# Optimization experiments

Hardware: AMD Instinct MI355X
Metric: run time of the kernel (lower is better)

The kernel has to match this reference:

```python
import jax, jax.numpy as jnp
import numpy as np

B, S, NH, HD = 2, 4096, 16, 64


def setup_inputs() -> dict:
    key = jax.random.key(0)
    kq, kk, kv = jax.random.split(key, 3)
    q = jax.random.normal(kq, (B, S, NH, HD), dtype=jnp.float32)
    k = jax.random.normal(kk, (B, S, NH, HD), dtype=jnp.float32)
    v = jax.random.normal(kv, (B, S, NH, HD), dtype=jnp.float32)
    return {"q": q, "k": k, "v": v}


def reference(q, k, v):
    # SDPA.__call__ with attention_mask=None, segment_ids=None, is_causal=True, dropout=identity
    q_len, nheads, kv_len = q.shape[-3], q.shape[-2], k.shape[-3]
    qs = q / jnp.sqrt(jnp.asarray(q.shape[-1], q.dtype))
    scores = jnp.einsum('...tnh,...snh->...tns', qs, k)  # [B, q, nheads, kv]
    # causal mask: tril over (q, kv), broadcast over heads axis (-2)
    causal = jnp.tril(jnp.ones((q_len, kv_len), dtype=jnp.bool_))[:, None, :]
    neg_inf = jnp.finfo(scores.dtype).min
    scores = jnp.where(causal, scores, neg_inf)
    weights = jax.nn.softmax(scores.astype(jnp.float32), axis=-1).astype(scores.dtype)
    attn = jnp.einsum('...tns,...snh->...tnh', weights, v)
    return attn
```

## Files before the change

### kernel.cpp

```cpp
#include <hip/hip_runtime.h>


constexpr int BATCH  = 2;
constexpr int SEQ    = 4096;
constexpr int NHEADS = 16;
constexpr int HDIM   = 64;
constexpr int ROWSTR = NHEADS * HDIM;
constexpr int BM     = 128;
constexpr int BN     = 64;
constexpr int QTILES = SEQ / BM;
constexpr int BH     = BATCH * NHEADS;

typedef __attribute__((ext_vector_type(8)))  short v8s;
typedef __attribute__((ext_vector_type(16))) float v16f;
typedef __attribute__((ext_vector_type(4)))  unsigned int v4u;
typedef __attribute__((ext_vector_type(2)))  unsigned int v2u;
typedef __attribute__((ext_vector_type(2)))  __bf16 v2bf;

__device__ __forceinline__ unsigned pkbf(float a, float b) {
#if __has_builtin(__builtin_amdgcn_cvt_pk_bf16_f32)
    return __builtin_bit_cast(unsigned, __builtin_amdgcn_cvt_pk_bf16_f32(a, b));
#else
    unsigned ua = __float_as_uint(a); ua += 0x7FFFu + ((ua >> 16) & 1u);
    unsigned ub = __float_as_uint(b); ub += 0x7FFFu + ((ub >> 16) & 1u);
    return (ua >> 16) | (ub & 0xFFFF0000u);
#endif
}

__device__ __forceinline__ int fswz(int r) { return (r & 7) ^ ((r >> 3) & 3); }

__device__ __forceinline__ void async16(const unsigned short* g, unsigned short* l) {
    __builtin_amdgcn_global_load_lds(
        (const __attribute__((address_space(1))) unsigned int*)g,
        (__attribute__((address_space(3))) unsigned int*)l, 16, 0, 0);
}

__global__ __launch_bounds__(256, 4)
void prep(const float* __restrict__ kf, const float* __restrict__ vf,
          unsigned short* __restrict__ kb, unsigned short* __restrict__ vt)
{
    __shared__ unsigned int lds[128 * 33];
    const int tid = threadIdx.x;
    const int blk = (int)blockIdx.x;

    if (blk < 1024) {
        const float4* src = (const float4*)kf + (size_t)blk * 2048;
        unsigned int* dst = (unsigned int*)kb + (size_t)blk * 4096;
        #pragma unroll
        for (int i = 0; i < 8; ++i) {
            const int n = i * 256 + tid;
            float4 f = src[n];
            *(v2u*)(dst + (size_t)n * 2) = (v2u){pkbf(f.x, f.y), pkbf(f.z, f.w)};
        }
        return;
    }

    const int t  = blk - 1024;
    const int b  = t >> 9;
    const int h  = (t >> 5) & 15;
    const int s0 = (t & 31) * 128;

    {
        const float4* vff = (const float4*)vf + (size_t)b * SEQ * 256;
        const int c2 = (tid & 15) * 2;
        #pragma unroll
        for (int i = 0; i < 8; ++i) {
            const int srow = i * 16 + (tid >> 4);
            float4 f = vff[(size_t)(s0 + srow) * 256 + h * 16 + (tid & 15)];
            lds[srow * 33 + c2]     = pkbf(f.x, f.y);
            lds[srow * 33 + c2 + 1] = pkbf(f.z, f.w);
        }
    }
    __syncthreads();
    {
        const int w    = tid >> 6;
        const int lane = tid & 63;
        const int sh   = (lane & 1) * 16;
        const unsigned int* lcol = &lds[w * 32 * 33 + (lane >> 1)];
        unsigned int out[16];
        #pragma unroll
        for (int j = 0; j < 16; ++j) {
            const unsigned a = lcol[(2 * j)     * 33];
            const unsigned c = lcol[(2 * j + 1) * 33];
            out[j] = ((a >> sh) & 0xFFFFu) | (((c >> sh) & 0xFFFFu) << 16);
        }
        unsigned int* dst = (unsigned int*)vt
            + ((size_t)((b * NHEADS + h) * HDIM + lane)) * (SEQ / 2)
            + ((s0 + w * 32) >> 1);
        #pragma unroll
        for (int j = 0; j < 4; ++j)
            *(v4u*)(dst + 4 * j) = (v4u){out[4*j], out[4*j+1], out[4*j+2], out[4*j+3]};
    }
}

__global__ __launch_bounds__(256, 4)
void fa_fwd(const float* __restrict__ qf, const unsigned short* __restrict__ kb,
            const unsigned short* __restrict__ vt, float* __restrict__ og)
{
    __shared__ __align__(16) unsigned short k_s[2][64 * 64];
    __shared__ __align__(16) unsigned short v_s[2][64 * 64];

    const int tid  = threadIdx.x;
    const int wave = tid >> 6;
    const int lane = tid & 63;
    const int hh   = lane >> 5;
    const int l32  = lane & 31;

    const int n  = (int)blockIdx.x;
    const int qtile = QTILES - 1 - (n >> 5);
    const int bh = n & 31;
    const int b = bh >> 4, h = bh & 15;
    const int qbase = qtile * BM;
    const int jmax  = 2 * qtile + 2;

    const int lrow  = lane >> 3;
    const int lcol8 = (lane & 7) ^ lrow ^ wave;
    const int fx = (l32 & 7) ^ ((l32 >> 3) & 3);

    {
        const int krow = tid >> 2;
        const int kc   = (tid & 3) * 16;
        const int sg0  = (2 * (tid & 3))     ^ fswz(krow);
        const int sg1  = (2 * (tid & 3) + 1) ^ fswz(krow);
        const float sc = 0.125f * 1.44269504088896340736f;
        #pragma unroll
        for (int half = 0; half < 2; ++half) {
            const float4* src = (const float4*)(qf +
                ((size_t)((b * SEQ + qbase + half * 64 + krow) * NHEADS + h)) * HDIM + kc);
            float4 f0 = src[0], f1 = src[1], f2 = src[2], f3 = src[3];
            unsigned short* dst = half ? &v_s[0][krow * 64] : &k_s[0][krow * 64];
            *(v4u*)&dst[sg0 * 8] = (v4u){pkbf(f0.x*sc, f0.y*sc), pkbf(f0.z*sc, f0.w*sc),
                                         pkbf(f1.x*sc, f1.y*sc), pkbf(f1.z*sc, f1.w*sc)};
            *(v4u*)&dst[sg1 * 8] = (v4u){pkbf(f2.x*sc, f2.y*sc), pkbf(f2.z*sc, f2.w*sc),
                                         pkbf(f3.x*sc, f3.y*sc), pkbf(f3.z*sc, f3.w*sc)};
        }
    }
    __syncthreads();
    v8s bq[4];
    {
        const int R = wave * 32 + l32;
        const unsigned short* qrow = (R < 64) ? &k_s[0][R * 64] : &v_s[0][(R - 64) * 64];
        #pragma unroll
        for (int c = 0; c < 4; ++c)
            bq[c] = *(const v8s*)&qrow[(((2*c + hh) ^ fswz(R & 63)) * 8)];
    }
    __syncthreads();

    const unsigned short* kgb = kb + (size_t)b * SEQ * ROWSTR + (size_t)h * HDIM;
    const unsigned short* vgb = vt + (size_t)bh * HDIM * SEQ;

    #pragma unroll
    for (int i = 0; i < 2; ++i) {
        const int rbase = i * 32 + wave * 8;
        async16(kgb + (size_t)(rbase + lrow) * ROWSTR + lcol8 * 8, &k_s[0][rbase * 64]);
        async16(vgb + (size_t)(rbase + lrow) * SEQ    + lcol8 * 8, &v_s[0][rbase * 64]);
    }

    v16f o_acc[2];
    o_acc[0] = (v16f)(0.f); o_acc[1] = (v16f)(0.f);
    float l_lane = 0.f;
    const int q_abs = qbase + wave * 32 + l32;

#if __has_builtin(__builtin_amdgcn_fdot2_f32_bf16)
    const v2bf ones2 = __builtin_bit_cast(v2bf, 0x3F803F80u);
#endif

    for (int jt = 0; jt < jmax; ++jt) {
        const int buf = jt & 1;
        __syncthreads();

        if (jt + 1 < jmax) {
            const int nb  = (jt + 1) & 1;
            const int kb2 = (jt + 1) * BN;
            #pragma unroll
            for (int i = 0; i < 2; ++i) {
                const int rbase = i * 32 + wave * 8;
                async16(kgb + (size_t)(kb2 + rbase + lrow) * ROWSTR + lcol8 * 8, &k_s[nb][rbase * 64]);
                async16(vgb + (size_t)(rbase + lrow) * SEQ + kb2    + lcol8 * 8, &v_s[nb][rbase * 64]);
            }
        }

        v16f sacc[2];
        sacc[0] = (v16f)(0.f); sacc[1] = (v16f)(0.f);
        __builtin_amdgcn_s_setprio(1);
        #pragma unroll
        for (int mt = 0; mt < 2; ++mt) {
            const int r = mt * 32 + l32;
            #pragma unroll
            for (int c = 0; c < 4; ++c) {
                v8s ak = *(const v8s*)&k_s[buf][r * 64 + (((2*c + hh) ^ fx) * 8)];
                sacc[mt] = __builtin_amdgcn_mfma_f32_32x32x16_bf16(ak, bq[c], sacc[mt], 0, 0, 0);
            }
        }
        __builtin_amdgcn_s_setprio(0);

        const bool masked = (jt >= jmax - 2);
        v8s pf[4];
        #pragma unroll
        for (int mt = 0; mt < 2; ++mt) {
            #pragma unroll
            for (int r = 0; r < 16; ++r) {
                float pv = __builtin_amdgcn_exp2f(sacc[mt][r]);
                if (masked) {
                    const int k_abs = jt * 64 + mt * 32 + (r & 3) + 8 * (r >> 2) + 4 * hh;
                    pv = (k_abs > q_abs) ? 0.f : pv;
                }
                sacc[mt][r] = pv;
#if !__has_builtin(__builtin_amdgcn_fdot2_f32_bf16)
                l_lane += pv;
#endif
            }
            #pragma unroll
            for (int cc = 0; cc < 2; ++cc) {
                const unsigned lo0 = pkbf(sacc[mt][8*cc+0], sacc[mt][8*cc+1]);
                const unsigned lo1 = pkbf(sacc[mt][8*cc+2], sacc[mt][8*cc+3]);
                const unsigned hi0 = pkbf(sacc[mt][8*cc+4], sacc[mt][8*cc+5]);
                const unsigned hi1 = pkbf(sacc[mt][8*cc+6], sacc[mt][8*cc+7]);
#if __has_builtin(__builtin_amdgcn_fdot2_f32_bf16)
                l_lane = __builtin_amdgcn_fdot2_f32_bf16(__builtin_bit_cast(v2bf, lo0), ones2, l_lane, false);
                l_lane = __builtin_amdgcn_fdot2_f32_bf16(__builtin_bit_cast(v2bf, lo1), ones2, l_lane, false);
                l_lane = __builtin_amdgcn_fdot2_f32_bf16(__builtin_bit_cast(v2bf, hi0), ones2, l_lane, false);
                l_lane = __builtin_amdgcn_fdot2_f32_bf16(__builtin_bit_cast(v2bf, hi1), ones2, l_lane, false);
#endif
#if __has_builtin(__builtin_amdgcn_permlane32_swap)
                auto r0 = __builtin_amdgcn_permlane32_swap(lo0, hi0, false, false);
                auto r1 = __builtin_amdgcn_permlane32_swap(lo1, hi1, false, false);
                pf[mt*2 + cc] = __builtin_bit_cast(v8s, (v4u){r0[0], r1[0], r0[1], r1[1]});
#else
                const unsigned s0 = hh ? lo0 : hi0;
                const unsigned s1 = hh ? lo1 : hi1;
                const unsigned t0 = (unsigned)__shfl_xor((int)s0, 32, 64);
                const unsigned t1 = (unsigned)__shfl_xor((int)s1, 32, 64);
                v4u w;
                w.x = hh ? t0 : lo0;
                w.y = hh ? t1 : lo1;
                w.z = hh ? hi0 : t0;
                w.w = hh ? hi1 : t1;
                pf[mt*2 + cc] = __builtin_bit_cast(v8s, w);
#endif
            }
        }

        __builtin_amdgcn_s_setprio(1);
        #pragma unroll
        for (int nt = 0; nt < 2; ++nt) {
            const int r = nt * 32 + l32;
            #pragma unroll
            for (int c = 0; c < 4; ++c) {
                v8s bv = *(const v8s*)&v_s[buf][r * 64 + (((2*c + hh) ^ fx) * 8)];
                o_acc[nt] = __builtin_amdgcn_mfma_f32_32x32x16_bf16(pf[c], bv, o_acc[nt], 0, 0, 0);
            }
        }
        __builtin_amdgcn_s_setprio(0);
    }

    const float lt = l_lane + __shfl_xor(l_lane, 32);

    #pragma unroll
    for (int r = 0; r < 16; ++r) {
        const int q_local = (r & 3) + 8 * (r >> 2) + 4 * hh;
        const float inv_l = 1.0f / __shfl(lt, q_local, 32);
        const int qrow = qbase + wave * 32 + q_local;
        float* dst = og + ((size_t)((b * SEQ + qrow) * NHEADS + h)) * HDIM + l32;
        dst[0]  = o_acc[0][r] * inv_l;
        dst[32] = o_acc[1][r] * inv_l;
    }
}

extern "C" void kernel_launch(void* const* d_in, const int* in_sizes, int n_in,
                              void* d_out, int out_size, void* d_ws, size_t ws_size,
                              hipStream_t stream) {
    const float* q = (const float*)d_in[0];
    const float* k = (const float*)d_in[1];
    const float* v = (const float*)d_in[2];
    float* out = (float*)d_out;

    const size_t TEN = (size_t)BATCH * NHEADS * SEQ * HDIM;
    unsigned short* kbuf = (unsigned short*)d_ws;
    unsigned short* vbuf = kbuf + TEN;

    prep<<<2048, 256, 0, stream>>>(k, v, kbuf, vbuf);
    fa_fwd<<<QTILES * BH, 256, 0, stream>>>(q, kbuf, vbuf, out);
}
```

Before: 242.6 us.

## Double query tile to 256 rows with 8 waves per block sharing K/V tiles

```diff
diff --git a/kernel.cpp b/kernel.cpp
--- a/kernel.cpp
+++ b/kernel.cpp
@@ -6,7 +6,7 @@
 constexpr int NHEADS = 16;
 constexpr int HDIM   = 64;
 constexpr int ROWSTR = NHEADS * HDIM;
-constexpr int BM     = 128;
+constexpr int BM     = 256;
 constexpr int BN     = 64;
 constexpr int QTILES = SEQ / BM;
 constexpr int BH     = BATCH * NHEADS;
@@ -93,7 +93,7 @@
     }
 }
 
-__global__ __launch_bounds__(256, 4)
+__global__ __launch_bounds__(512, 2)
 void fa_fwd(const float* __restrict__ qf, const unsigned short* __restrict__ kb,
             const unsigned short* __restrict__ vt, float* __restrict__ og)
 {
@@ -111,24 +111,30 @@
     const int bh = n & 31;
     const int b = bh >> 4, h = bh & 15;
     const int qbase = qtile * BM;
-    const int jmax  = 2 * qtile + 2;
+    const int jmax  = 4 * qtile + 4;
 
     const int lrow  = lane >> 3;
-    const int lcol8 = (lane & 7) ^ lrow ^ wave;
+    const int lcol8 = (lane & 7) ^ lrow ^ (wave & 3);
     const int fx = (l32 & 7) ^ ((l32 >> 3) & 3);
 
     {
         const int krow = tid >> 2;
         const int kc   = (tid & 3) * 16;
-        const int sg0  = (2 * (tid & 3))     ^ fswz(krow);
-        const int sg1  = (2 * (tid & 3) + 1) ^ fswz(krow);
         const float sc = 0.125f * 1.44269504088896340736f;
         #pragma unroll
         for (int half = 0; half < 2; ++half) {
+            const int row = half * 128 + krow;
+            const int rr  = row & 63;
+            const int sg0 = (2 * (tid & 3))     ^ fswz(rr);
+            const int sg1 = (2 * (tid & 3) + 1) ^ fswz(rr);
             const float4* src = (const float4*)(qf +
-                ((size_t)((b * SEQ + qbase + half * 64 + krow) * NHEADS + h)) * HDIM + kc);
+                ((size_t)((b * SEQ + qbase + row) * NHEADS + h)) * HDIM + kc);
             float4 f0 = src[0], f1 = src[1], f2 = src[2], f3 = src[3];
-            unsigned short* dst = half ? &v_s[0][krow * 64] : &k_s[0][krow * 64];
+            const int sel = row >> 6;
+            unsigned short* dst = (sel == 0) ? &k_s[0][rr * 64]
+                                : (sel == 1) ? &k_s[1][rr * 64]
+                                : (sel == 2) ? &v_s[0][rr * 64]
+                                             : &v_s[1][rr * 64];
             *(v4u*)&dst[sg0 * 8] = (v4u){pkbf(f0.x*sc, f0.y*sc), pkbf(f0.z*sc, f0.w*sc),
                                          pkbf(f1.x*sc, f1.y*sc), pkbf(f1.z*sc, f1.w*sc)};
             *(v4u*)&dst[sg1 * 8] = (v4u){pkbf(f2.x*sc, f2.y*sc), pkbf(f2.z*sc, f2.w*sc),
@@ -138,24 +144,29 @@
     __syncthreads();
     v8s bq[4];
     {
-        const int R = wave * 32 + l32;
-        const unsigned short* qrow = (R < 64) ? &k_s[0][R * 64] : &v_s[0][(R - 64) * 64];
+        const int R   = wave * 32 + l32;
+        const int sel = wave >> 1;
+        const int rr  = R & 63;
+        const unsigned short* qb = (sel == 0) ? &k_s[0][0]
+                                 : (sel == 1) ? &k_s[1][0]
+                                 : (sel == 2) ? &v_s[0][0]
+                                              : &v_s[1][0];
         #pragma unroll
         for (int c = 0; c < 4; ++c)
-            bq[c] = *(const v8s*)&qrow[(((2*c + hh) ^ fswz(R & 63)) * 8)];
+            bq[c] = *(const v8s*)&qb[rr * 64 + (((2*c + hh) ^ fswz(rr)) * 8)];
     }
     __syncthreads();
 
     const unsigned short* kgb = kb + (size_t)b * SEQ * ROWSTR + (size_t)h * HDIM;
     const unsigned short* vgb = vt + (size_t)bh * HDIM * SEQ;
 
-    #pragma unroll
-    for (int i = 0; i < 2; ++i) {
-        const int rbase = i * 32 + wave * 8;
+    {
+        const int rbase = wave * 8;
         async16(kgb + (size_t)(rbase + lrow) * ROWSTR + lcol8 * 8, &k_s[0][rbase * 64]);
         async16(vgb + (size_t)(rbase + lrow) * SEQ    + lcol8 * 8, &v_s[0][rbase * 64]);
     }
 
+    const v16f vzero = (v16f)(0.f);
     v16f o_acc[2];
     o_acc[0] = (v16f)(0.f); o_acc[1] = (v16f)(0.f);
     float l_lane = 0.f;
@@ -172,29 +183,29 @@
         if (jt + 1 < jmax) {
             const int nb  = (jt + 1) & 1;
             const int kb2 = (jt + 1) * BN;
-            #pragma unroll
-            for (int i = 0; i < 2; ++i) {
-                const int rbase = i * 32 + wave * 8;
-                async16(kgb + (size_t)(kb2 + rbase + lrow) * ROWSTR + lcol8 * 8, &k_s[nb][rbase * 64]);
-                async16(vgb + (size_t)(rbase + lrow) * SEQ + kb2    + lcol8 * 8, &v_s[nb][rbase * 64]);
-            }
+            const int rbase = wave * 8;
+            async16(kgb + (size_t)(kb2 + rbase + lrow) * ROWSTR + lcol8 * 8, &k_s[nb][rbase * 64]);
+            async16(vgb + (size_t)(rbase + lrow) * SEQ + kb2    + lcol8 * 8, &v_s[nb][rbase * 64]);
         }
 
         v16f sacc[2];
-        sacc[0] = (v16f)(0.f); sacc[1] = (v16f)(0.f);
         __builtin_amdgcn_s_setprio(1);
         #pragma unroll
         for (int mt = 0; mt < 2; ++mt) {
             const int r = mt * 32 + l32;
-            #pragma unroll
-            for (int c = 0; c < 4; ++c) {
+            {
+                v8s ak = *(const v8s*)&k_s[buf][r * 64 + ((hh ^ fx) * 8)];
+                sacc[mt] = __builtin_amdgcn_mfma_f32_32x32x16_bf16(ak, bq[0], vzero, 0, 0, 0);
+            }
+            #pragma unroll
+            for (int c = 1; c < 4; ++c) {
                 v8s ak = *(const v8s*)&k_s[buf][r * 64 + (((2*c + hh) ^ fx) * 8)];
                 sacc[mt] = __builtin_amdgcn_mfma_f32_32x32x16_bf16(ak, bq[c], sacc[mt], 0, 0, 0);
             }
         }
         __builtin_amdgcn_s_setprio(0);
 
-        const bool masked = (jt >= jmax - 2);
+        const bool masked = (jt >= jmax - 4);
         v8s pf[4];
         #pragma unroll
         for (int mt = 0; mt < 2; ++mt) {
@@ -280,5 +291,5 @@
     unsigned short* vbuf = kbuf + TEN;
 
     prep<<<2048, 256, 0, stream>>>(k, v, kbuf, vbuf);
-    fa_fwd<<<QTILES * BH, 256, 0, stream>>>(q, kbuf, vbuf, out);
-}
+    fa_fwd<<<QTILES * BH, 512, 0, stream>>>(q, kbuf, vbuf, out);
+}
```

Result: slower. 260.0 us (+7.2%).

## Triple-buffer K/V tiles with prefetch distance two and single barrier per step

Applied to the files above, without the earlier changes.

```diff
diff --git a/kernel.cpp b/kernel.cpp
--- a/kernel.cpp
+++ b/kernel.cpp
@@ -97,8 +97,8 @@
 void fa_fwd(const float* __restrict__ qf, const unsigned short* __restrict__ kb,
             const unsigned short* __restrict__ vt, float* __restrict__ og)
 {
-    __shared__ __align__(16) unsigned short k_s[2][64 * 64];
-    __shared__ __align__(16) unsigned short v_s[2][64 * 64];
+    __shared__ __align__(16) unsigned short k_s[3][64 * 64];
+    __shared__ __align__(16) unsigned short v_s[3][64 * 64];
 
     const int tid  = threadIdx.x;
     const int wave = tid >> 6;
@@ -150,12 +150,20 @@
     const unsigned short* vgb = vt + (size_t)bh * HDIM * SEQ;
 
     #pragma unroll
-    for (int i = 0; i < 2; ++i) {
-        const int rbase = i * 32 + wave * 8;
-        async16(kgb + (size_t)(rbase + lrow) * ROWSTR + lcol8 * 8, &k_s[0][rbase * 64]);
-        async16(vgb + (size_t)(rbase + lrow) * SEQ    + lcol8 * 8, &v_s[0][rbase * 64]);
-    }
-
+    for (int t = 0; t < 2; ++t) {
+        const int kb2 = t * BN;
+        #pragma unroll
+        for (int i = 0; i < 2; ++i) {
+            const int rbase = i * 32 + wave * 8;
+            async16(kgb + (size_t)(kb2 + rbase + lrow) * ROWSTR + lcol8 * 8, &k_s[t][rbase * 64]);
+            async16(vgb + (size_t)(rbase + lrow) * SEQ + kb2    + lcol8 * 8, &v_s[t][rbase * 64]);
+        }
+    }
+    asm volatile("s_waitcnt vmcnt(4)" ::: "memory");
+    __builtin_amdgcn_s_barrier();
+    __builtin_amdgcn_sched_barrier(0);
+
+    const v16f vzero = (v16f)(0.f);
     v16f o_acc[2];
     o_acc[0] = (v16f)(0.f); o_acc[1] = (v16f)(0.f);
     float l_lane = 0.f;
@@ -165,37 +173,40 @@
     const v2bf ones2 = __builtin_bit_cast(v2bf, 0x3F803F80u);
 #endif
 
+    int cur = 0;
     for (int jt = 0; jt < jmax; ++jt) {
-        const int buf = jt & 1;
-        __syncthreads();
-
-        if (jt + 1 < jmax) {
-            const int nb  = (jt + 1) & 1;
-            const int kb2 = (jt + 1) * BN;
+        if (jt + 2 < jmax) {
+            int pf = cur + 2; if (pf >= 3) pf -= 3;
+            const int kb2 = (jt + 2) * BN;
             #pragma unroll
             for (int i = 0; i < 2; ++i) {
                 const int rbase = i * 32 + wave * 8;
-                async16(kgb + (size_t)(kb2 + rbase + lrow) * ROWSTR + lcol8 * 8, &k_s[nb][rbase * 64]);
-                async16(vgb + (size_t)(rbase + lrow) * SEQ + kb2    + lcol8 * 8, &v_s[nb][rbase * 64]);
-            }
-        }
-
+                async16(kgb + (size_t)(kb2 + rbase + lrow) * ROWSTR + lcol8 * 8, &k_s[pf][rbase * 64]);
+                async16(vgb + (size_t)(rbase + lrow) * SEQ + kb2    + lcol8 * 8, &v_s[pf][rbase * 64]);
+            }
+        }
+
+        const unsigned short* ksb = &k_s[cur][0];
+        const unsigned short* vsb = &v_s[cur][0];
         v16f sacc[2];
-        sacc[0] = (v16f)(0.f); sacc[1] = (v16f)(0.f);
         __builtin_amdgcn_s_setprio(1);
         #pragma unroll
         for (int mt = 0; mt < 2; ++mt) {
             const int r = mt * 32 + l32;
-            #pragma unroll
-            for (int c = 0; c < 4; ++c) {
-                v8s ak = *(const v8s*)&k_s[buf][r * 64 + (((2*c + hh) ^ fx) * 8)];
+            {
+                v8s ak = *(const v8s*)&ksb[r * 64 + ((hh ^ fx) * 8)];
+                sacc[mt] = __builtin_amdgcn_mfma_f32_32x32x16_bf16(ak, bq[0], vzero, 0, 0, 0);
+            }
+            #pragma unroll
+            for (int c = 1; c < 4; ++c) {
+                v8s ak = *(const v8s*)&ksb[r * 64 + (((2*c + hh) ^ fx) * 8)];
                 sacc[mt] = __builtin_amdgcn_mfma_f32_32x32x16_bf16(ak, bq[c], sacc[mt], 0, 0, 0);
             }
         }
         __builtin_amdgcn_s_setprio(0);
 
         const bool masked = (jt >= jmax - 2);
-        v8s pf[4];
+        v8s pf4[4];
         #pragma unroll
         for (int mt = 0; mt < 2; ++mt) {
             #pragma unroll
@@ -225,7 +236,7 @@
 #if __has_builtin(__builtin_amdgcn_permlane32_swap)
                 auto r0 = __builtin_amdgcn_permlane32_swap(lo0, hi0, false, false);
                 auto r1 = __builtin_amdgcn_permlane32_swap(lo1, hi1, false, false);
-                pf[mt*2 + cc] = __builtin_bit_cast(v8s, (v4u){r0[0], r1[0], r0[1], r1[1]});
+                pf4[mt*2 + cc] = __builtin_bit_cast(v8s, (v4u){r0[0], r1[0], r0[1], r1[1]});
 #else
                 const unsigned s0 = hh ? lo0 : hi0;
                 const unsigned s1 = hh ? lo1 : hi1;
@@ -236,7 +247,7 @@
                 w.y = hh ? t1 : lo1;
                 w.z = hh ? hi0 : t0;
                 w.w = hh ? hi1 : t1;
-                pf[mt*2 + cc] = __builtin_bit_cast(v8s, w);
+                pf4[mt*2 + cc] = __builtin_bit_cast(v8s, w);
 #endif
             }
         }
@@ -247,11 +258,19 @@
             const int r = nt * 32 + l32;
             #pragma unroll
             for (int c = 0; c < 4; ++c) {
-                v8s bv = *(const v8s*)&v_s[buf][r * 64 + (((2*c + hh) ^ fx) * 8)];
-                o_acc[nt] = __builtin_amdgcn_mfma_f32_32x32x16_bf16(pf[c], bv, o_acc[nt], 0, 0, 0);
+                v8s bv = *(const v8s*)&vsb[r * 64 + (((2*c + hh) ^ fx) * 8)];
+                o_acc[nt] = __builtin_amdgcn_mfma_f32_32x32x16_bf16(pf4[c], bv, o_acc[nt], 0, 0, 0);
             }
         }
         __builtin_amdgcn_s_setprio(0);
+
+        if (jt + 1 < jmax) {
+            if (jt + 2 < jmax) asm volatile("s_waitcnt vmcnt(4)" ::: "memory");
+            else               asm volatile("s_waitcnt vmcnt(0)" ::: "memory");
+            __builtin_amdgcn_s_barrier();
+            __builtin_amdgcn_sched_barrier(0);
+        }
+        cur = (cur == 2) ? 0 : cur + 1;
     }
 
     const float lt = l_lane + __shfl_xor(l_lane, 32);
```

Measured after the change: 246.9 us. Within noise of the previous version (+1.7%).
